# Optimization experiments

Hardware: AMD Instinct MI355X
Metric: run time of the kernel (lower is better)

## Reference

```python
import jax, jax.numpy as jnp
import numpy as np


def _conv(x, w, b, stride, pad):
    y = jax.lax.conv_general_dilated(
        x, w, (stride, stride), [(pad, pad), (pad, pad)],
        dimension_numbers=('NCHW', 'OIHW', 'NCHW'))
    return y + b[None, :, None, None]


def _maxpool(x):
    # kernel 3, stride 2, padding 1 (torch MaxPool2d semantics)
    return jax.lax.reduce_window(
        x, -jnp.inf, jax.lax.max,
        (1, 1, 3, 3), (1, 1, 2, 2), [(0, 0), (0, 0), (1, 1), (1, 1)])


def _squash(s, eps=1e-8):
    n2 = jnp.sum(s * s, axis=-1, keepdims=True)
    return s * (n2 / (1.0 + n2)) / jnp.sqrt(n2 + eps)


def setup_inputs() -> dict:
    key = jax.random.key(0)
    ks = jax.random.split(key, 17)
    s = 0.05
    inp = {
        'x': jax.random.normal(ks[0], (128, 3, 32, 32), jnp.float32),
        'cw1': jax.random.normal(ks[1], (96, 3, 3, 3), jnp.float32) * s,
        'cb1': jnp.zeros((96,), jnp.float32),
        'cw2': jax.random.normal(ks[2], (256, 96, 3, 3), jnp.float32) * s,
        'cb2': jnp.zeros((256,), jnp.float32),
        'cw3': jax.random.normal(ks[3], (384, 256, 3, 3), jnp.float32) * s,
        'cb3': jnp.zeros((384,), jnp.float32),
        'pw': jax.random.normal(ks[4], (256, 384, 3, 3), jnp.float32) * s,  # 32 caps * 8 dim
        'pb': jnp.zeros((256,), jnp.float32),
        'Wcaps': jax.random.normal(ks[5], (100, 1152, 16, 8), jnp.float32) * s,
        'fw1': jax.random.normal(ks[6], (1600, 4096), jnp.float32) * s,
        'fb1': jnp.zeros((4096,), jnp.float32),
        'fw2': jax.random.normal(ks[7], (4096, 4096), jnp.float32) * s,
        'fb2': jnp.zeros((4096,), jnp.float32),
        'fw3': jax.random.normal(ks[8], (4096, 100), jnp.float32) * s,
        'fb3': jnp.zeros((100,), jnp.float32),
    }
    return inp


def reference(x, cw1, cb1, cw2, cb2, cw3, cb3, pw, pb, Wcaps,
              fw1, fb1, fw2, fb2, fw3, fb3):
    ROUTINGS = 3
    # AlexNet-style conv backbone
    h = jax.nn.relu(_conv(x, cw1, cb1, 1, 1))   # [B,96,32,32]
    h = _maxpool(h)                              # [B,96,16,16]
    h = jax.nn.relu(_conv(h, cw2, cb2, 1, 1))   # [B,256,16,16]
    h = _maxpool(h)                              # [B,256,8,8]
    h = jax.nn.relu(_conv(h, cw3, cb3, 1, 1))   # [B,384,8,8]
    # PrimaryCaps: conv 384 -> 32*8, k3 s1 p0 -> [B,256,6,6]
    p = _conv(h, pw, pb, 1, 0)
    u = _squash(p.reshape(p.shape[0], -1, 8))   # [B,1152,8]
    # DenseCapsule: x_hat[b,o,i,d] = sum_e W[o,i,d,e] * u[b,i,e]
    x_hat = jnp.einsum('oide,bie->boid', Wcaps, u)  # [B,100,1152,16]
    x_hat_d = jax.lax.stop_gradient(x_hat)
    b = jnp.zeros(x_hat.shape[:3], x_hat.dtype)     # [B,100,1152]
    v = None
    for r in range(ROUTINGS):
        c = jax.nn.softmax(b, axis=1)               # couple over out caps
        if r == ROUTINGS - 1:
            v = _squash(jnp.einsum('boi,boid->bod', c, x_hat))
        else:
            v = _squash(jnp.einsum('boi,boid->bod', c, x_hat_d))
            b = b + jnp.einsum('boid,bod->boi', x_hat_d, v)
    # Flatten + FC head (dropout is identity at eval)
    f = v.reshape(v.shape[0], -1)                   # [B,1600]
    f = jax.nn.relu(f @ fw1 + fb1)
    f = jax.nn.relu(f @ fw2 + fb2)
    return f @ fw3 + fb3                            # [B,100]
```

## Files before the change

### kernel.cpp

```cpp
#include <hip/hip_runtime.h>
#include <cstddef>


typedef __attribute__((ext_vector_type(8))) short bf8_t;
typedef __attribute__((ext_vector_type(4))) float f4_t;

__device__ inline void cvt_hilo8(const float* f, unsigned* h, unsigned* l)
{
  #pragma unroll
  for (int j = 0; j < 4; ++j) {
    unsigned u0 = __float_as_uint(f[2 * j]);
    unsigned u1 = __float_as_uint(f[2 * j + 1]);
    h[j] = (u0 >> 16) | (u1 & 0xFFFF0000u);
    float r0 = f[2 * j]     - __uint_as_float(u0 & 0xFFFF0000u);
    float r1 = f[2 * j + 1] - __uint_as_float(u1 & 0xFFFF0000u);
    l[j] = (__float_as_uint(r0) >> 16) | (__float_as_uint(r1) & 0xFFFF0000u);
  }
}

__global__ __launch_bounds__(256) void conv1_k(
    const float* __restrict__ x, const float* __restrict__ wt,
    const float* __restrict__ bias, float* __restrict__ out)
{
  int idx = blockIdx.x * 256 + threadIdx.x;
  int w = idx & 31, h = (idx >> 5) & 31, b = idx >> 10;
  int co0 = blockIdx.y * 24;

  float xv[27];
  const float* xb = x + (size_t)b * 3072;
  #pragma unroll
  for (int ci = 0; ci < 3; ++ci)
    #pragma unroll
    for (int dh = 0; dh < 3; ++dh) {
      int ih = h + dh - 1;
      #pragma unroll
      for (int dw = 0; dw < 3; ++dw) {
        int iw = w + dw - 1;
        bool ok = ((unsigned)ih < 32u) & ((unsigned)iw < 32u);
        xv[ci * 9 + dh * 3 + dw] = ok ? xb[(ci << 10) + (ih << 5) + iw] : 0.f;
      }
    }

  float* op = out + (size_t)b * 98304 + ((size_t)co0 << 10) + (h << 5) + w;
  const float* wp = wt + (size_t)co0 * 27;
  #pragma unroll 2
  for (int co = 0; co < 24; ++co) {
    float acc = bias[co0 + co];
    #pragma unroll
    for (int k = 0; k < 27; ++k)
      acc += xv[k] * wp[co * 27 + k];
    op[(size_t)co << 10] = fmaxf(acc, 0.f);
  }
}

__global__ __launch_bounds__(256) void maxpool_k(
    const float* __restrict__ in, float* __restrict__ out, int H)
{
  int Ho = H >> 1;
  int idx = blockIdx.x * 256 + threadIdx.x;
  int wo = idx % Ho;
  int t2 = idx / Ho;
  int ho = t2 % Ho;
  int bc = t2 / Ho;
  const float* ip = in + (size_t)bc * H * H;
  float m = -3.4e38f;
  #pragma unroll
  for (int dh = 0; dh < 3; ++dh) {
    int ih = 2 * ho - 1 + dh;
    if (ih < 0 || ih >= H) continue;
    #pragma unroll
    for (int dw = 0; dw < 3; ++dw) {
      int iw = 2 * wo - 1 + dw;
      if (iw < 0 || iw >= H) continue;
      m = fmaxf(m, ip[ih * H + iw]);
    }
  }
  out[idx] = m;
}

template <int CI, int H, int PAD, int WO, bool SPLIT>
__global__ __launch_bounds__(256) void convgemm_mfma(
    const float* __restrict__ in, const float* __restrict__ wt,
    const float* __restrict__ bias, float* __restrict__ out,
    int CO, int relu, int KC)
{
  constexpr int K = CI * 9;
  constexpr int NPIX = WO * WO;
  __shared__ uint4 Ah[256], Al[256], Bh[256], Bl[256];
  int n0 = blockIdx.x * 64, m0 = blockIdx.y * 64;
  int kbeg = SPLIT ? blockIdx.z * KC : 0;
  int kend = SPLIT ? kbeg + KC : K;
  int t = threadIdx.x;
  int lane = t & 63;
  int wave = __builtin_amdgcn_readfirstlane(t >> 6);
  int wm = wave & 1, wn = wave >> 1;
  int lr = lane & 15, lq = lane >> 4;
  int smA = t >> 2, sgA = t & 3;

  int nn = n0 + lane;
  int bb = nn / NPIX, xy = nn - bb * NPIX;
  int ho = xy / WO, wo = xy - ho * WO;
  int ih0 = ho - PAD, iw0 = wo - PAD;
  const float* inb = in + (size_t)bb * CI * H * H;

  float fa[8], fb[8];
  auto loadA = [&](int k0) {
    const float4* ap = (const float4*)(wt + (size_t)(m0 + smA) * K + k0 + sgA * 8);
    float4 a0 = ap[0], a1 = ap[1];
    fa[0] = a0.x; fa[1] = a0.y; fa[2] = a0.z; fa[3] = a0.w;
    fa[4] = a1.x; fa[5] = a1.y; fa[6] = a1.z; fa[7] = a1.w;
  };
  auto loadB = [&](int k0) {
    int kb = k0 + wave * 8;
    int ci = kb / 9, rr = kb - ci * 9;
    int dh = rr / 3, dw = rr - dh * 3;
    #pragma unroll
    for (int j = 0; j < 8; ++j) {
      int ih = ih0 + dh, iw = iw0 + dw;
      bool ok = (ih >= 0 && ih < H && iw >= 0 && iw < H);
      fb[j] = ok ? inb[(ci * H + ih) * H + iw] : 0.f;
      if (++dw == 3) { dw = 0; if (++dh == 3) { dh = 0; ++ci; } }
    }
  };

  loadA(kbeg); loadB(kbeg);
  f4_t acc[2][2];
  #pragma unroll
  for (int mt = 0; mt < 2; ++mt)
    #pragma unroll
    for (int nt = 0; nt < 2; ++nt) acc[mt][nt] = (f4_t)0.0f;

  for (int k0 = kbeg; k0 < kend; k0 += 32) {
    if (k0 > kbeg) __syncthreads();
    unsigned ha[4], la[4], hb[4], lb[4];
    cvt_hilo8(fa, ha, la);
    cvt_hilo8(fb, hb, lb);
    Ah[sgA * 64 + smA] = make_uint4(ha[0], ha[1], ha[2], ha[3]);
    Al[sgA * 64 + smA] = make_uint4(la[0], la[1], la[2], la[3]);
    Bh[wave * 64 + lane] = make_uint4(hb[0], hb[1], hb[2], hb[3]);
    Bl[wave * 64 + lane] = make_uint4(lb[0], lb[1], lb[2], lb[3]);
    __syncthreads();
    if (k0 + 32 < kend) { loadA(k0 + 32); loadB(k0 + 32); }
    bf8_t av_h[2], av_l[2], bv_h[2], bv_l[2];
    #pragma unroll
    for (int mt = 0; mt < 2; ++mt) {
      int ui = lq * 64 + wm * 32 + mt * 16 + lr;
      av_h[mt] = *(const bf8_t*)&Ah[ui];
      av_l[mt] = *(const bf8_t*)&Al[ui];
    }
    #pragma unroll
    for (int nt = 0; nt < 2; ++nt) {
      int ui = lq * 64 + wn * 32 + nt * 16 + lr;
      bv_h[nt] = *(const bf8_t*)&Bh[ui];
      bv_l[nt] = *(const bf8_t*)&Bl[ui];
    }
    #pragma unroll
    for (int mt = 0; mt < 2; ++mt)
      #pragma unroll
      for (int nt = 0; nt < 2; ++nt) {
        acc[mt][nt] = __builtin_amdgcn_mfma_f32_16x16x32_bf16(av_h[mt], bv_h[nt], acc[mt][nt], 0, 0, 0);
        acc[mt][nt] = __builtin_amdgcn_mfma_f32_16x16x32_bf16(av_h[mt], bv_l[nt], acc[mt][nt], 0, 0, 0);
        acc[mt][nt] = __builtin_amdgcn_mfma_f32_16x16x32_bf16(av_l[mt], bv_h[nt], acc[mt][nt], 0, 0, 0);
      }
  }
  #pragma unroll
  for (int mt = 0; mt < 2; ++mt)
    #pragma unroll
    for (int nt = 0; nt < 2; ++nt) {
      #pragma unroll
      for (int r = 0; r < 4; ++r) {
        int m = m0 + wm * 32 + mt * 16 + lq * 4 + r;
        int n = n0 + wn * 32 + nt * 16 + lr;
        int b = n / NPIX, pxy = n - b * NPIX;
        size_t oidx = ((size_t)b * CO + m) * NPIX + pxy;
        if (SPLIT) {
          atomicAdd(out + oidx, acc[mt][nt][r]);
        } else {
          float vv = acc[mt][nt][r] + bias[m];
          if (relu) vv = fmaxf(vv, 0.f);
          out[oidx] = vv;
        }
      }
    }
}

__global__ __launch_bounds__(256) void fc_mfma(
    const float* __restrict__ A, const float* __restrict__ W,
    float* __restrict__ C, int K, int N, int KC)
{
  __shared__ uint4 Ah[256], Al[256], Bh[256], Bl[256];
  int n0 = blockIdx.x * 64, m0 = blockIdx.y * 64;
  int kbeg = blockIdx.z * KC, kend = kbeg + KC;
  int t = threadIdx.x;
  int lane = t & 63;
  int wave = __builtin_amdgcn_readfirstlane(t >> 6);
  int wm = wave & 1, wn = wave >> 1;
  int lr = lane & 15, lq = lane >> 4;
  int smA = t >> 2, sgA = t & 3;

  float fa[8], fb[8];
  auto loadA = [&](int k0) {
    const float4* ap = (const float4*)(A + (size_t)(m0 + smA) * K + k0 + sgA * 8);
    float4 a0 = ap[0], a1 = ap[1];
    fa[0] = a0.x; fa[1] = a0.y; fa[2] = a0.z; fa[3] = a0.w;
    fa[4] = a1.x; fa[5] = a1.y; fa[6] = a1.z; fa[7] = a1.w;
  };
  auto loadB = [&](int k0) {
    const float* wp = W + (size_t)(k0 + wave * 8) * N + n0 + lane;
    #pragma unroll
    for (int j = 0; j < 8; ++j) fb[j] = wp[(size_t)j * N];
  };

  loadA(kbeg); loadB(kbeg);
  f4_t acc[2][2];
  #pragma unroll
  for (int mt = 0; mt < 2; ++mt)
    #pragma unroll
    for (int nt = 0; nt < 2; ++nt) acc[mt][nt] = (f4_t)0.0f;

  for (int k0 = kbeg; k0 < kend; k0 += 32) {
    if (k0 > kbeg) __syncthreads();
    unsigned ha[4], la[4], hb[4], lb[4];
    cvt_hilo8(fa, ha, la);
    cvt_hilo8(fb, hb, lb);
    Ah[sgA * 64 + smA] = make_uint4(ha[0], ha[1], ha[2], ha[3]);
    Al[sgA * 64 + smA] = make_uint4(la[0], la[1], la[2], la[3]);
    Bh[wave * 64 + lane] = make_uint4(hb[0], hb[1], hb[2], hb[3]);
    Bl[wave * 64 + lane] = make_uint4(lb[0], lb[1], lb[2], lb[3]);
    __syncthreads();
    if (k0 + 32 < kend) { loadA(k0 + 32); loadB(k0 + 32); }
    bf8_t av_h[2], av_l[2], bv_h[2], bv_l[2];
    #pragma unroll
    for (int mt = 0; mt < 2; ++mt) {
      int ui = lq * 64 + wm * 32 + mt * 16 + lr;
      av_h[mt] = *(const bf8_t*)&Ah[ui];
      av_l[mt] = *(const bf8_t*)&Al[ui];
    }
    #pragma unroll
    for (int nt = 0; nt < 2; ++nt) {
      int ui = lq * 64 + wn * 32 + nt * 16 + lr;
      bv_h[nt] = *(const bf8_t*)&Bh[ui];
      bv_l[nt] = *(const bf8_t*)&Bl[ui];
    }
    #pragma unroll
    for (int mt = 0; mt < 2; ++mt)
      #pragma unroll
      for (int nt = 0; nt < 2; ++nt) {
        acc[mt][nt] = __builtin_amdgcn_mfma_f32_16x16x32_bf16(av_h[mt], bv_h[nt], acc[mt][nt], 0, 0, 0);
        acc[mt][nt] = __builtin_amdgcn_mfma_f32_16x16x32_bf16(av_h[mt], bv_l[nt], acc[mt][nt], 0, 0, 0);
        acc[mt][nt] = __builtin_amdgcn_mfma_f32_16x16x32_bf16(av_l[mt], bv_h[nt], acc[mt][nt], 0, 0, 0);
      }
  }
  #pragma unroll
  for (int mt = 0; mt < 2; ++mt)
    #pragma unroll
    for (int nt = 0; nt < 2; ++nt) {
      #pragma unroll
      for (int r = 0; r < 4; ++r) {
        int m = m0 + wm * 32 + mt * 16 + lq * 4 + r;
        int n = n0 + wn * 32 + nt * 16 + lr;
        atomicAdd(C + (size_t)m * N + n, acc[mt][nt][r]);
      }
    }
}

__global__ __launch_bounds__(256) void squash8_k(
    const float* __restrict__ p, const float* __restrict__ pb,
    float* __restrict__ ut)
{
  int idx = blockIdx.x * 256 + threadIdx.x;
  if (idx >= 147456) return;
  int b = idx & 127, i = idx >> 7;
  const float4* pp = (const float4*)(p + ((size_t)b * 1152 + i) * 8);
  float4 a = pp[0], bb = pp[1];
  float pv[8] = {a.x, a.y, a.z, a.w, bb.x, bb.y, bb.z, bb.w};
  int f0 = i * 8;
  #pragma unroll
  for (int e = 0; e < 8; ++e) pv[e] += pb[(f0 + e) / 36];
  float n2 = 0.f;
  #pragma unroll
  for (int e = 0; e < 8; ++e) n2 += pv[e] * pv[e];
  float sc = (n2 / (1.f + n2)) * rsqrtf(n2 + 1e-8f);
  #pragma unroll
  for (int e = 0; e < 8; ++e)
    ut[(size_t)i * 1024 + e * 128 + b] = pv[e] * sc;
}

__global__ __launch_bounds__(256) void caps_squash16(
    const float* __restrict__ s, float* __restrict__ v, float* __restrict__ vt)
{
  int idx = blockIdx.x * 256 + threadIdx.x;
  if (idx >= 12800) return;
  int b = idx / 100, o = idx % 100;
  const float4* sp = (const float4*)(s + (size_t)idx * 16);
  float4 a = sp[0], bb = sp[1], c = sp[2], d = sp[3];
  float n2 = a.x * a.x + a.y * a.y + a.z * a.z + a.w * a.w +
             bb.x * bb.x + bb.y * bb.y + bb.z * bb.z + bb.w * bb.w +
             c.x * c.x + c.y * c.y + c.z * c.z + c.w * c.w +
             d.x * d.x + d.y * d.y + d.z * d.z + d.w * d.w;
  float sc = (n2 / (1.f + n2)) * rsqrtf(n2 + 1e-8f);
  float vv[16] = {a.x, a.y, a.z, a.w, bb.x, bb.y, bb.z, bb.w,
                  c.x, c.y, c.z, c.w, d.x, d.y, d.z, d.w};
  float4* vp = (float4*)(v + (size_t)idx * 16);
  float4 o0 = {vv[0] * sc, vv[1] * sc, vv[2] * sc, vv[3] * sc};
  float4 o1 = {vv[4] * sc, vv[5] * sc, vv[6] * sc, vv[7] * sc};
  float4 o2 = {vv[8] * sc, vv[9] * sc, vv[10] * sc, vv[11] * sc};
  float4 o3 = {vv[12] * sc, vv[13] * sc, vv[14] * sc, vv[15] * sc};
  vp[0] = o0; vp[1] = o1; vp[2] = o2; vp[3] = o3;
  #pragma unroll
  for (int dd = 0; dd < 16; ++dd)
    vt[((size_t)o * 16 + dd) * 128 + b] = vv[dd] * sc;
}

__global__ __launch_bounds__(256) void caps_spass_mfma(
    const float* __restrict__ W, const float* __restrict__ ut,
    const float* __restrict__ ct, float* __restrict__ s, int uniform)
{
  __shared__ uint4 Ah[512], Al[512];
  int o = blockIdx.x, ks = blockIdx.y;
  int t = threadIdx.x;
  int lane = t & 63;
  int wave = __builtin_amdgcn_readfirstlane(t >> 6);
  int lr = lane & 15, lq = lane >> 4;
  int b = t & 127, half = t >> 7;
  int i0 = ks * 144;

  float fu[16], fc[2], fw[8];
  auto loadUC = [&](int j) {
    int ib = i0 + j * 4 + half * 2;
    #pragma unroll
    for (int q = 0; q < 2; ++q) {
      int i = ib + q;
      #pragma unroll
      for (int e = 0; e < 8; ++e)
        fu[q * 8 + e] = ut[(size_t)i * 1024 + e * 128 + b];
      fc[q] = uniform ? 0.01f : ct[((size_t)o * 1152 + i) * 128 + b];
    }
  };
  auto loadW = [&](int j) {
    int i = i0 + j * 4 + lq;
    const float4* wp = (const float4*)(W + (((size_t)o * 1152 + i) * 16 + lr) * 8);
    float4 w0 = wp[0], w1 = wp[1];
    fw[0] = w0.x; fw[1] = w0.y; fw[2] = w0.z; fw[3] = w0.w;
    fw[4] = w1.x; fw[5] = w1.y; fw[6] = w1.z; fw[7] = w1.w;
  };

  loadUC(0); loadW(0);
  f4_t acc[2];
  acc[0] = (f4_t)0.0f; acc[1] = (f4_t)0.0f;

  for (int j = 0; j < 36; ++j) {
    float cu[16];
    #pragma unroll
    for (int q = 0; q < 2; ++q)
      #pragma unroll
      for (int e = 0; e < 8; ++e)
        cu[q * 8 + e] = fc[q] * fu[q * 8 + e];
    unsigned h0[4], l0[4], h1[4], l1[4], wh[4], wl[4];
    cvt_hilo8(cu, h0, l0);
    cvt_hilo8(cu + 8, h1, l1);
    cvt_hilo8(fw, wh, wl);
    uint4 uwh = make_uint4(wh[0], wh[1], wh[2], wh[3]);
    uint4 uwl = make_uint4(wl[0], wl[1], wl[2], wl[3]);
    bf8_t bfh = *(const bf8_t*)&uwh;
    bf8_t bfl = *(const bf8_t*)&uwl;
    if (j > 0) __syncthreads();
    Ah[(half * 2 + 0) * 128 + b] = make_uint4(h0[0], h0[1], h0[2], h0[3]);
    Al[(half * 2 + 0) * 128 + b] = make_uint4(l0[0], l0[1], l0[2], l0[3]);
    Ah[(half * 2 + 1) * 128 + b] = make_uint4(h1[0], h1[1], h1[2], h1[3]);
    Al[(half * 2 + 1) * 128 + b] = make_uint4(l1[0], l1[1], l1[2], l1[3]);
    __syncthreads();
    if (j + 1 < 36) { loadUC(j + 1); loadW(j + 1); }
    #pragma unroll
    for (int mt = 0; mt < 2; ++mt) {
      int bidx = wave * 16 + mt * 64 + lr;
      bf8_t avh = *(const bf8_t*)&Ah[lq * 128 + bidx];
      bf8_t avl = *(const bf8_t*)&Al[lq * 128 + bidx];
      acc[mt] = __builtin_amdgcn_mfma_f32_16x16x32_bf16(avh, bfh, acc[mt], 0, 0, 0);
      acc[mt] = __builtin_amdgcn_mfma_f32_16x16x32_bf16(avh, bfl, acc[mt], 0, 0, 0);
      acc[mt] = __builtin_amdgcn_mfma_f32_16x16x32_bf16(avl, bfh, acc[mt], 0, 0, 0);
    }
  }
  #pragma unroll
  for (int mt = 0; mt < 2; ++mt)
    #pragma unroll
    for (int r = 0; r < 4; ++r) {
      int bb = wave * 16 + mt * 64 + lq * 4 + r;
      atomicAdd(s + ((size_t)bb * 100 + o) * 16 + lr, acc[mt][r]);
    }
}

__global__ __launch_bounds__(256) void caps_bupdate(
    const float* __restrict__ W, const float* __restrict__ ut,
    const float* __restrict__ vt, float* __restrict__ blogt, int accum)
{
  __shared__ __align__(16) float Wt[64 * 160];
  int o = blockIdx.x, ic = blockIdx.y;
  int t = threadIdx.x;
  int lane = t & 63;
  int wave = __builtin_amdgcn_readfirstlane(t >> 6);
  int lr = lane & 15, lq = lane >> 4;
  int dhalf = (lq & 1) << 3;
  int hl = lq >> 1;

  {
    const float4* Wg = (const float4*)(W + ((size_t)o * 1152 + (size_t)ic * 64) * 128);
    for (int l = t; l < 2048; l += 256) {
      float4 w = Wg[l];
      int li = l >> 5;
      int rem = l & 31;
      int d = rem >> 1;
      int e0 = (rem & 1) << 2;
      float* dst = &Wt[li * 160 + e0 * 20 + d];
      dst[0] = w.x; dst[20] = w.y; dst[40] = w.z; dst[60] = w.w;
    }
  }

  bf8_t B1[8], B2[8];
  #pragma unroll
  for (int nt = 0; nt < 8; ++nt) {
    int b = nt * 16 + lr;
    float vv[8];
    #pragma unroll
    for (int j = 0; j < 8; ++j)
      vv[j] = vt[((size_t)o * 16 + dhalf + j) * 128 + b];
    unsigned h[4], l2[4];
    cvt_hilo8(vv, h, l2);
    uint4 uh = make_uint4(h[0], h[1], h[2], h[3]);
    uint4 ul = (lq < 2) ? make_uint4(l2[0], l2[1], l2[2], l2[3])
                        : make_uint4(0u, 0u, 0u, 0u);
    B1[nt] = *(const bf8_t*)&uh;
    B2[nt] = *(const bf8_t*)&ul;
  }
  __syncthreads();

  unsigned lomask = hl ? 0xFFFF0000u : 0u;

  for (int mi = 0; mi < 8; ++mi) {
    int mt = wave * 8 + mi;
    int liA = mt * 2 + (lr >> 3);
    int eA = lr & 7;
    const float* wp = &Wt[liA * 160 + eA * 20 + dhalf];
    float4 wa = *(const float4*)wp;
    float4 wb = *(const float4*)(wp + 4);
    float fw[8] = {wa.x, wa.y, wa.z, wa.w, wb.x, wb.y, wb.z, wb.w};
    unsigned ha[4];
    #pragma unroll
    for (int j = 0; j < 4; ++j) {
      float f0 = fw[2 * j], f1 = fw[2 * j + 1];
      f0 -= __uint_as_float(__float_as_uint(f0) & lomask);
      f1 -= __uint_as_float(__float_as_uint(f1) & lomask);
      ha[j] = (__float_as_uint(f0) >> 16) | (__float_as_uint(f1) & 0xFFFF0000u);
    }
    uint4 ua = make_uint4(ha[0], ha[1], ha[2], ha[3]);
    bf8_t A = *(const bf8_t*)&ua;

    int gi = ic * 64 + mt * 2 + hl;
    const float* up = ut + (size_t)gi * 1024 + (size_t)(((lq & 1) << 2)) * 128;
    #pragma unroll
    for (int nt = 0; nt < 8; ++nt) {
      f4_t acc = (f4_t)0.0f;
      acc = __builtin_amdgcn_mfma_f32_16x16x32_bf16(A, B1[nt], acc, 0, 0, 0);
      acc = __builtin_amdgcn_mfma_f32_16x16x32_bf16(A, B2[nt], acc, 0, 0, 0);
      int b = nt * 16 + lr;
      float p = acc[0] * up[b] + acc[1] * up[128 + b] +
                acc[2] * up[256 + b] + acc[3] * up[384 + b];
      p += __shfl_xor(p, 16);
      if (!(lq & 1)) {
        size_t off = ((size_t)o * 1152 + gi) * 128 + b;
        if (accum) blogt[off] += p; else blogt[off] = p;
      }
    }
  }
}

__global__ __launch_bounds__(256) void caps_softmax(
    const float* __restrict__ blogt, float* __restrict__ ct)
{
  int idx = blockIdx.x * 256 + threadIdx.x;
  if (idx >= 147456) return;
  const float* bp = blogt + idx;
  float m = -3.4e38f;
  for (int o = 0; o < 100; ++o) m = fmaxf(m, bp[(size_t)o * 147456]);
  float sum = 0.f;
  for (int o = 0; o < 100; ++o) sum += __expf(bp[(size_t)o * 147456] - m);
  float inv = 1.f / sum;
  for (int o = 0; o < 100; ++o)
    ct[(size_t)o * 147456 + idx] = __expf(bp[(size_t)o * 147456] - m) * inv;
}

__global__ __launch_bounds__(256) void bias_act_k(
    float* __restrict__ C, const float* __restrict__ bias, int N, int total, int relu)
{
  int idx = blockIdx.x * 256 + threadIdx.x;
  if (idx >= total) return;
  float vv = C[idx] + bias[idx % N];
  if (relu) vv = fmaxf(vv, 0.f);
  C[idx] = vv;
}

__global__ __launch_bounds__(128) void fc3_seed(
    const float* __restrict__ bias, float* __restrict__ out)
{
  int idx = blockIdx.x * 128 + threadIdx.x;
  if (idx < 12800) out[idx] = bias[idx % 100];
}

__global__ __launch_bounds__(128) void fc3_sk(
    const float* __restrict__ A, const float* __restrict__ W,
    float* __restrict__ out)
{
  __shared__ float Al[1024];
  int m = blockIdx.x, z = blockIdx.y, t = threadIdx.x;
  int kbeg = z * 1024;
  const float* ap = A + (size_t)m * 4096 + kbeg;
  for (int l = t; l < 1024; l += 128) Al[l] = ap[l];
  __syncthreads();
  if (t < 100) {
    float acc = 0.f;
    const float* wp = W + (size_t)kbeg * 100 + t;
    #pragma unroll 8
    for (int k = 0; k < 1024; ++k) acc += Al[k] * wp[(size_t)k * 100];
    atomicAdd(out + m * 100 + t, acc);
  }
}

extern "C" void kernel_launch(void* const* d_in, const int* in_sizes, int n_in,
                              void* d_out, int out_size, void* d_ws, size_t ws_size,
                              hipStream_t stream)
{
  (void)in_sizes; (void)n_in; (void)out_size; (void)ws_size;
  const float* x   = (const float*)d_in[0];
  const float* cw1 = (const float*)d_in[1];
  const float* cb1 = (const float*)d_in[2];
  const float* cw2 = (const float*)d_in[3];
  const float* cb2 = (const float*)d_in[4];
  const float* cw3 = (const float*)d_in[5];
  const float* cb3 = (const float*)d_in[6];
  const float* pw  = (const float*)d_in[7];
  const float* pb  = (const float*)d_in[8];
  const float* Wc  = (const float*)d_in[9];
  const float* fw1 = (const float*)d_in[10];
  const float* fb1 = (const float*)d_in[11];
  const float* fw2 = (const float*)d_in[12];
  const float* fb2 = (const float*)d_in[13];
  const float* fw3 = (const float*)d_in[14];
  const float* fb3 = (const float*)d_in[15];
  float* ws = (float*)d_ws;

  const size_t OFF_A  = 0;
  const size_t OFF_B  = 12582912;
  const size_t OFF_U  = 15728640;
  const size_t OFF_P  = 16908288;
  const size_t OFF_C  = 18087936;
  const size_t OFF_V  = 32833536;
  const size_t OFF_S  = 33038336;
  const size_t OFF_F1 = 33243136;
  const size_t OFF_F2 = 33767424;

  float* A     = ws + OFF_A;
  float* Bf    = ws + OFF_B;
  float* ut    = ws + OFF_U;
  float* p     = ws + OFF_P;
  float* vt    = ws + OFF_P;
  float* ct    = ws + OFF_C;
  float* v     = ws + OFF_V;
  float* s     = ws + OFF_S;
  float* f1    = ws + OFF_F1;
  float* f2    = ws + OFF_F2;
  float* blogt = ws + OFF_A;

  hipMemsetAsync(p,  0, (size_t)1179648 * 4, stream);
  hipMemsetAsync(f1, 0, (size_t)524288 * 4, stream);
  hipMemsetAsync(f2, 0, (size_t)524288 * 4, stream);

  conv1_k<<<dim3(512, 4), 256, 0, stream>>>(x, cw1, cb1, A);
  maxpool_k<<<12288, 256, 0, stream>>>(A, Bf, 32);
  convgemm_mfma<96, 16, 1, 16, false><<<dim3(512, 4), 256, 0, stream>>>(Bf, cw2, cb2, A, 256, 1, 0);
  maxpool_k<<<8192, 256, 0, stream>>>(A, Bf, 16);
  convgemm_mfma<256, 8, 1, 8, false><<<dim3(128, 6), 256, 0, stream>>>(Bf, cw3, cb3, A, 384, 1, 0);
  convgemm_mfma<384, 8, 0, 6, true><<<dim3(72, 4, 2), 256, 0, stream>>>(A, pw, pb, p, 256, 0, 1728);
  squash8_k<<<576, 256, 0, stream>>>(p, pb, ut);

  for (int r = 0; r < 3; ++r) {
    hipMemsetAsync(s, 0, (size_t)204800 * 4, stream);
    if (r == 0) {
      caps_spass_mfma<<<dim3(100, 8), 256, 0, stream>>>(Wc, ut, ut , s, 1);
    } else {
      caps_softmax<<<576, 256, 0, stream>>>(blogt, ct);
      caps_spass_mfma<<<dim3(100, 8), 256, 0, stream>>>(Wc, ut, ct, s, 0);
    }
    caps_squash16<<<50, 256, 0, stream>>>(s, v, vt);
    if (r < 2)
      caps_bupdate<<<dim3(100, 18), 256, 0, stream>>>(Wc, ut, vt, blogt, r);
  }

  fc_mfma<<<dim3(64, 2, 2), 256, 0, stream>>>(v,  fw1, f1, 1600, 4096, 800);
  bias_act_k<<<2048, 256, 0, stream>>>(f1, fb1, 4096, 524288, 1);
  fc_mfma<<<dim3(64, 2, 4), 256, 0, stream>>>(f1, fw2, f2, 4096, 4096, 1024);
  bias_act_k<<<2048, 256, 0, stream>>>(f2, fb2, 4096, 524288, 1);
  fc3_seed<<<100, 128, 0, stream>>>(fb3, (float*)d_out);
  fc3_sk<<<dim3(128, 4), 128, 0, stream>>>(f2, fw3, (float*)d_out);
}
```

Before: 1.045 ms.

## Switch conv backbone to NHWC with pre-split bf16 hi/lo activations and weights

Conv activations are now stored in NHWC layout as separate bf16 high and low halves, and the conv weights are pre-split into hi/lo bf16 with a reordered K index of (tap, channel). Each conv GEMM can then load its A and B tiles with 16-byte vector loads instead of 8 scattered scalar loads, and it no longer converts fp32 to hi/lo in the inner loop. Maxpool and squash are adapted to the new layout. The cost is three extra weight-split kernels per call and a more complex epilogue that writes 2-byte hi/lo outputs.

```diff
diff --git a/kernel.cpp b/kernel.cpp
--- a/kernel.cpp
+++ b/kernel.cpp
@@ -18,9 +18,37 @@
   }
 }
 
+__device__ inline void split1(float f, unsigned short& h, unsigned short& l)
+{
+  unsigned u = __float_as_uint(f);
+  h = (unsigned short)(u >> 16);
+  float r = f - __uint_as_float(u & 0xFFFF0000u);
+  l = (unsigned short)(__float_as_uint(r) >> 16);
+}
+
+__device__ inline float bf2f(unsigned short h, unsigned short l)
+{
+  return __uint_as_float((unsigned)h << 16) + __uint_as_float((unsigned)l << 16);
+}
+
+__global__ __launch_bounds__(256) void wsplit_k(
+    const float* __restrict__ w, unsigned short* __restrict__ oh,
+    unsigned short* __restrict__ ol, int CO, int CI)
+{
+  int idx = blockIdx.x * 256 + threadIdx.x;
+  int ci = idx % CI;
+  int t2 = idx / CI;
+  int r = t2 % 9, co = t2 / 9;
+  float f = w[((size_t)co * CI + ci) * 9 + r];
+  unsigned short h, l;
+  split1(f, h, l);
+  oh[idx] = h; ol[idx] = l;
+}
+
 __global__ __launch_bounds__(256) void conv1_k(
     const float* __restrict__ x, const float* __restrict__ wt,
-    const float* __restrict__ bias, float* __restrict__ out)
+    const float* __restrict__ bias, unsigned short* __restrict__ oh,
+    unsigned short* __restrict__ ol)
 {
   int idx = blockIdx.x * 256 + threadIdx.x;
   int w = idx & 31, h = (idx >> 5) & 31, b = idx >> 10;
@@ -41,47 +69,61 @@
       }
     }
 
-  float* op = out + (size_t)b * 98304 + ((size_t)co0 << 10) + (h << 5) + w;
+  size_t obase = ((size_t)b * 1024 + (h << 5) + w) * 96 + co0;
   const float* wp = wt + (size_t)co0 * 27;
   #pragma unroll 2
-  for (int co = 0; co < 24; ++co) {
-    float acc = bias[co0 + co];
-    #pragma unroll
-    for (int k = 0; k < 27; ++k)
-      acc += xv[k] * wp[co * 27 + k];
-    op[(size_t)co << 10] = fmaxf(acc, 0.f);
-  }
-}
-
-__global__ __launch_bounds__(256) void maxpool_k(
-    const float* __restrict__ in, float* __restrict__ out, int H)
-{
-  int Ho = H >> 1;
+  for (int cp = 0; cp < 12; ++cp) {
+    float a0 = bias[co0 + 2 * cp], a1 = bias[co0 + 2 * cp + 1];
+    #pragma unroll
+    for (int k = 0; k < 27; ++k) {
+      a0 += xv[k] * wp[(2 * cp) * 27 + k];
+      a1 += xv[k] * wp[(2 * cp + 1) * 27 + k];
+    }
+    a0 = fmaxf(a0, 0.f); a1 = fmaxf(a1, 0.f);
+    unsigned short h0, l0, h1, l1;
+    split1(a0, h0, l0); split1(a1, h1, l1);
+    *(unsigned*)(oh + obase + 2 * cp) = (unsigned)h0 | ((unsigned)h1 << 16);
+    *(unsigned*)(ol + obase + 2 * cp) = (unsigned)l0 | ((unsigned)l1 << 16);
+  }
+}
+
+template <int C, int H>
+__global__ __launch_bounds__(256) void maxpool_bf(
+    const unsigned short* __restrict__ inh, const unsigned short* __restrict__ inl,
+    unsigned short* __restrict__ outh, unsigned short* __restrict__ outl)
+{
+  constexpr int Ho = H >> 1;
   int idx = blockIdx.x * 256 + threadIdx.x;
-  int wo = idx % Ho;
-  int t2 = idx / Ho;
-  int ho = t2 % Ho;
-  int bc = t2 / Ho;
-  const float* ip = in + (size_t)bc * H * H;
-  float m = -3.4e38f;
+  int c = idx % C;
+  int q = idx / C;
+  int wo = q % Ho;
+  int q2 = q / Ho;
+  int ho = q2 % Ho, b = q2 / Ho;
+  float best = -3.4e38f;
+  unsigned short bh = 0, bl = 0;
   #pragma unroll
   for (int dh = 0; dh < 3; ++dh) {
     int ih = 2 * ho - 1 + dh;
-    if (ih < 0 || ih >= H) continue;
+    if ((unsigned)ih >= (unsigned)H) continue;
     #pragma unroll
     for (int dw = 0; dw < 3; ++dw) {
       int iw = 2 * wo - 1 + dw;
-      if (iw < 0 || iw >= H) continue;
-      m = fmaxf(m, ip[ih * H + iw]);
-    }
-  }
-  out[idx] = m;
+      if ((unsigned)iw >= (unsigned)H) continue;
+      size_t off = ((size_t)(b * H + ih) * H + iw) * C + c;
+      unsigned short uh = inh[off], ul = inl[off];
+      float f = bf2f(uh, ul);
+      if (f > best) { best = f; bh = uh; bl = ul; }
+    }
+  }
+  outh[idx] = bh; outl[idx] = bl;
 }
 
 template <int CI, int H, int PAD, int WO, bool SPLIT>
-__global__ __launch_bounds__(256) void convgemm_mfma(
-    const float* __restrict__ in, const float* __restrict__ wt,
-    const float* __restrict__ bias, float* __restrict__ out,
+__global__ __launch_bounds__(256) void convgemm_nhwc(
+    const unsigned short* __restrict__ inh, const unsigned short* __restrict__ inl,
+    const unsigned short* __restrict__ wh, const unsigned short* __restrict__ wl,
+    const float* __restrict__ bias, unsigned short* __restrict__ outh,
+    unsigned short* __restrict__ outl, float* __restrict__ outf,
     int CO, int relu, int KC)
 {
   constexpr int K = CI * 9;
@@ -95,32 +137,117 @@
   int wave = __builtin_amdgcn_readfirstlane(t >> 6);
   int wm = wave & 1, wn = wave >> 1;
   int lr = lane & 15, lq = lane >> 4;
-  int smA = t >> 2, sgA = t & 3;
-
-  int nn = n0 + lane;
-  int bb = nn / NPIX, xy = nn - bb * NPIX;
+
+  int nn = m0 + lane;
+  int bpix = nn / NPIX, xy = nn - bpix * NPIX;
   int ho = xy / WO, wo = xy - ho * WO;
   int ih0 = ho - PAD, iw0 = wo - PAD;
-  const float* inb = in + (size_t)bb * CI * H * H;
+  size_t ibase = (size_t)bpix * H * H;
+
+  uint4 a_h, a_l, b_h, b_l;
+  auto loadA = [&](int k0) {
+    int kk = k0 + wave * 8;
+    int r = kk / CI, ci0 = kk - r * CI;
+    int dh = r / 3, dw = r - dh * 3;
+    int ih = ih0 + dh, iw = iw0 + dw;
+    bool ok = ((unsigned)ih < (unsigned)H) & ((unsigned)iw < (unsigned)H);
+    if (ok) {
+      size_t ad = ((ibase + (size_t)ih * H + iw) * CI + ci0);
+      a_h = *(const uint4*)(inh + ad);
+      a_l = *(const uint4*)(inl + ad);
+    } else {
+      a_h = make_uint4(0u, 0u, 0u, 0u);
+      a_l = make_uint4(0u, 0u, 0u, 0u);
+    }
+  };
+  auto loadB = [&](int k0) {
+    int kk = k0 + wave * 8;
+    size_t ad = (size_t)(n0 + lane) * K + kk;
+    b_h = *(const uint4*)(wh + ad);
+    b_l = *(const uint4*)(wl + ad);
+  };
+
+  loadA(kbeg); loadB(kbeg);
+  f4_t acc[2][2];
+  #pragma unroll
+  for (int mt = 0; mt < 2; ++mt)
+    #pragma unroll
+    for (int nt = 0; nt < 2; ++nt) acc[mt][nt] = (f4_t)0.0f;
+
+  for (int k0 = kbeg; k0 < kend; k0 += 32) {
+    if (k0 > kbeg) __syncthreads();
+    Ah[t] = a_h; Al[t] = a_l; Bh[t] = b_h; Bl[t] = b_l;
+    __syncthreads();
+    if (k0 + 32 < kend) { loadA(k0 + 32); loadB(k0 + 32); }
+    bf8_t av_h[2], av_l[2], bv_h[2], bv_l[2];
+    #pragma unroll
+    for (int mt = 0; mt < 2; ++mt) {
+      int ui = lq * 64 + wm * 32 + mt * 16 + lr;
+      av_h[mt] = *(const bf8_t*)&Ah[ui];
+      av_l[mt] = *(const bf8_t*)&Al[ui];
+    }
+    #pragma unroll
+    for (int nt = 0; nt < 2; ++nt) {
+      int ui = lq * 64 + wn * 32 + nt * 16 + lr;
+      bv_h[nt] = *(const bf8_t*)&Bh[ui];
+      bv_l[nt] = *(const bf8_t*)&Bl[ui];
+    }
+    #pragma unroll
+    for (int mt = 0; mt < 2; ++mt)
+      #pragma unroll
+      for (int nt = 0; nt < 2; ++nt) {
+        acc[mt][nt] = __builtin_amdgcn_mfma_f32_16x16x32_bf16(av_h[mt], bv_h[nt], acc[mt][nt], 0, 0, 0);
+        acc[mt][nt] = __builtin_amdgcn_mfma_f32_16x16x32_bf16(av_h[mt], bv_l[nt], acc[mt][nt], 0, 0, 0);
+        acc[mt][nt] = __builtin_amdgcn_mfma_f32_16x16x32_bf16(av_l[mt], bv_h[nt], acc[mt][nt], 0, 0, 0);
+      }
+  }
+  #pragma unroll
+  for (int mt = 0; mt < 2; ++mt)
+    #pragma unroll
+    for (int nt = 0; nt < 2; ++nt) {
+      #pragma unroll
+      for (int r = 0; r < 4; ++r) {
+        int m = m0 + wm * 32 + mt * 16 + lq * 4 + r;
+        int n = n0 + wn * 32 + nt * 16 + lr;
+        size_t oidx = (size_t)m * CO + n;
+        if (SPLIT) {
+          atomicAdd(outf + oidx, acc[mt][nt][r]);
+        } else {
+          float vv = acc[mt][nt][r] + bias[n];
+          if (relu) vv = fmaxf(vv, 0.f);
+          unsigned short h, l;
+          split1(vv, h, l);
+          outh[oidx] = h; outl[oidx] = l;
+        }
+      }
+    }
+}
+
+__global__ __launch_bounds__(256) void fc_mfma(
+    const float* __restrict__ A, const float* __restrict__ W,
+    float* __restrict__ C, int K, int N, int KC)
+{
+  __shared__ uint4 Ah[256], Al[256], Bh[256], Bl[256];
+  int n0 = blockIdx.x * 64, m0 = blockIdx.y * 64;
+  int kbeg = blockIdx.z * KC, kend = kbeg + KC;
+  int t = threadIdx.x;
+  int lane = t & 63;
+  int wave = __builtin_amdgcn_readfirstlane(t >> 6);
+  int wm = wave & 1, wn = wave >> 1;
+  int lr = lane & 15, lq = lane >> 4;
+  int smA = t >> 2, sgA = t & 3;
 
   float fa[8], fb[8];
   auto loadA = [&](int k0) {
-    const float4* ap = (const float4*)(wt + (size_t)(m0 + smA) * K + k0 + sgA * 8);
+    const float4* ap = (const float4*)(A + (size_t)(m0 + smA) * K + k0 + sgA * 8);
     float4 a0 = ap[0], a1 = ap[1];
     fa[0] = a0.x; fa[1] = a0.y; fa[2] = a0.z; fa[3] = a0.w;
     fa[4] = a1.x; fa[5] = a1.y; fa[6] = a1.z; fa[7] = a1.w;
   };
   auto loadB = [&](int k0) {
-    int kb = k0 + wave * 8;
-    int ci = kb / 9, rr = kb - ci * 9;
-    int dh = rr / 3, dw = rr - dh * 3;
-    #pragma unroll
-    for (int j = 0; j < 8; ++j) {
-      int ih = ih0 + dh, iw = iw0 + dw;
-      bool ok = (ih >= 0 && ih < H && iw >= 0 && iw < H);
-      fb[j] = ok ? inb[(ci * H + ih) * H + iw] : 0.f;
-      if (++dw == 3) { dw = 0; if (++dh == 3) { dh = 0; ++ci; } }
-    }
+    const float* wp = W + (size_t)(k0 + wave * 8) * N + n0 + lane;
+    #pragma unroll
+    for (int j = 0; j < 8; ++j) fb[j] = wp[(size_t)j * N];
   };
 
   loadA(kbeg); loadB(kbeg);
@@ -171,94 +298,6 @@
       for (int r = 0; r < 4; ++r) {
         int m = m0 + wm * 32 + mt * 16 + lq * 4 + r;
         int n = n0 + wn * 32 + nt * 16 + lr;
-        int b = n / NPIX, pxy = n - b * NPIX;
-        size_t oidx = ((size_t)b * CO + m) * NPIX + pxy;
-        if (SPLIT) {
-          atomicAdd(out + oidx, acc[mt][nt][r]);
-        } else {
-          float vv = acc[mt][nt][r] + bias[m];
-          if (relu) vv = fmaxf(vv, 0.f);
-          out[oidx] = vv;
-        }
-      }
-    }
-}
-
-__global__ __launch_bounds__(256) void fc_mfma(
-    const float* __restrict__ A, const float* __restrict__ W,
-    float* __restrict__ C, int K, int N, int KC)
-{
-  __shared__ uint4 Ah[256], Al[256], Bh[256], Bl[256];
-  int n0 = blockIdx.x * 64, m0 = blockIdx.y * 64;
-  int kbeg = blockIdx.z * KC, kend = kbeg + KC;
-  int t = threadIdx.x;
-  int lane = t & 63;
-  int wave = __builtin_amdgcn_readfirstlane(t >> 6);
-  int wm = wave & 1, wn = wave >> 1;
-  int lr = lane & 15, lq = lane >> 4;
-  int smA = t >> 2, sgA = t & 3;
-
-  float fa[8], fb[8];
-  auto loadA = [&](int k0) {
-    const float4* ap = (const float4*)(A + (size_t)(m0 + smA) * K + k0 + sgA * 8);
-    float4 a0 = ap[0], a1 = ap[1];
-    fa[0] = a0.x; fa[1] = a0.y; fa[2] = a0.z; fa[3] = a0.w;
-    fa[4] = a1.x; fa[5] = a1.y; fa[6] = a1.z; fa[7] = a1.w;
-  };
-  auto loadB = [&](int k0) {
-    const float* wp = W + (size_t)(k0 + wave * 8) * N + n0 + lane;
-    #pragma unroll
-    for (int j = 0; j < 8; ++j) fb[j] = wp[(size_t)j * N];
-  };
-
-  loadA(kbeg); loadB(kbeg);
-  f4_t acc[2][2];
-  #pragma unroll
-  for (int mt = 0; mt < 2; ++mt)
-    #pragma unroll
-    for (int nt = 0; nt < 2; ++nt) acc[mt][nt] = (f4_t)0.0f;
-
-  for (int k0 = kbeg; k0 < kend; k0 += 32) {
-    if (k0 > kbeg) __syncthreads();
-    unsigned ha[4], la[4], hb[4], lb[4];
-    cvt_hilo8(fa, ha, la);
-    cvt_hilo8(fb, hb, lb);
-    Ah[sgA * 64 + smA] = make_uint4(ha[0], ha[1], ha[2], ha[3]);
-    Al[sgA * 64 + smA] = make_uint4(la[0], la[1], la[2], la[3]);
-    Bh[wave * 64 + lane] = make_uint4(hb[0], hb[1], hb[2], hb[3]);
-    Bl[wave * 64 + lane] = make_uint4(lb[0], lb[1], lb[2], lb[3]);
-    __syncthreads();
-    if (k0 + 32 < kend) { loadA(k0 + 32); loadB(k0 + 32); }
-    bf8_t av_h[2], av_l[2], bv_h[2], bv_l[2];
-    #pragma unroll
-    for (int mt = 0; mt < 2; ++mt) {
-      int ui = lq * 64 + wm * 32 + mt * 16 + lr;
-      av_h[mt] = *(const bf8_t*)&Ah[ui];
-      av_l[mt] = *(const bf8_t*)&Al[ui];
-    }
-    #pragma unroll
-    for (int nt = 0; nt < 2; ++nt) {
-      int ui = lq * 64 + wn * 32 + nt * 16 + lr;
-      bv_h[nt] = *(const bf8_t*)&Bh[ui];
-      bv_l[nt] = *(const bf8_t*)&Bl[ui];
-    }
-    #pragma unroll
-    for (int mt = 0; mt < 2; ++mt)
-      #pragma unroll
-      for (int nt = 0; nt < 2; ++nt) {
-        acc[mt][nt] = __builtin_amdgcn_mfma_f32_16x16x32_bf16(av_h[mt], bv_h[nt], acc[mt][nt], 0, 0, 0);
-        acc[mt][nt] = __builtin_amdgcn_mfma_f32_16x16x32_bf16(av_h[mt], bv_l[nt], acc[mt][nt], 0, 0, 0);
-        acc[mt][nt] = __builtin_amdgcn_mfma_f32_16x16x32_bf16(av_l[mt], bv_h[nt], acc[mt][nt], 0, 0, 0);
-      }
-  }
-  #pragma unroll
-  for (int mt = 0; mt < 2; ++mt)
-    #pragma unroll
-    for (int nt = 0; nt < 2; ++nt) {
-      #pragma unroll
-      for (int r = 0; r < 4; ++r) {
-        int m = m0 + wm * 32 + mt * 16 + lq * 4 + r;
-        int n = n0 + wn * 32 + nt * 16 + lr;
         atomicAdd(C + (size_t)m * N + n, acc[mt][nt][r]);
       }
     }
@@ -271,12 +310,13 @@
   int idx = blockIdx.x * 256 + threadIdx.x;
   if (idx >= 147456) return;
   int b = idx & 127, i = idx >> 7;
-  const float4* pp = (const float4*)(p + ((size_t)b * 1152 + i) * 8);
-  float4 a = pp[0], bb = pp[1];
-  float pv[8] = {a.x, a.y, a.z, a.w, bb.x, bb.y, bb.z, bb.w};
-  int f0 = i * 8;
-  #pragma unroll
-  for (int e = 0; e < 8; ++e) pv[e] += pb[(f0 + e) / 36];
+  float pv[8];
+  #pragma unroll
+  for (int e = 0; e < 8; ++e) {
+    int f = i * 8 + e;
+    int co = f / 36, pix = f - co * 36;
+    pv[e] = p[((size_t)b * 36 + pix) * 256 + co] + pb[co];
+  }
   float n2 = 0.f;
   #pragma unroll
   for (int e = 0; e < 8; ++e) n2 += pv[e] * pv[e];
@@ -558,8 +598,6 @@
   const size_t OFF_F1 = 33243136;
   const size_t OFF_F2 = 33767424;
 
-  float* A     = ws + OFF_A;
-  float* Bf    = ws + OFF_B;
   float* ut    = ws + OFF_U;
   float* p     = ws + OFF_P;
   float* vt    = ws + OFF_P;
@@ -570,16 +608,41 @@
   float* f2    = ws + OFF_F2;
   float* blogt = ws + OFF_A;
 
+  unsigned short* h1h  = (unsigned short*)(ws + OFF_A);
+  unsigned short* h1l  = h1h + 12582912;
+  unsigned short* mp1h = (unsigned short*)(ws + OFF_B);
+  unsigned short* mp1l = mp1h + 3145728;
+  unsigned short* h2h  = (unsigned short*)(ws + OFF_A);
+  unsigned short* h2l  = h2h + 8388608;
+  unsigned short* mp2h = (unsigned short*)(ws + OFF_B);
+  unsigned short* mp2l = mp2h + 2097152;
+  unsigned short* h3h  = (unsigned short*)(ws + OFF_A);
+  unsigned short* h3l  = h3h + 3145728;
+
+  unsigned short* wc2h = (unsigned short*)(ws + OFF_C);
+  unsigned short* wc2l = wc2h + 221184;
+  unsigned short* wc3h = wc2l + 221184;
+  unsigned short* wc3l = wc3h + 884736;
+  unsigned short* pwth = wc3l + 884736;
+  unsigned short* pwtl = pwth + 884736;
+
   hipMemsetAsync(p,  0, (size_t)1179648 * 4, stream);
   hipMemsetAsync(f1, 0, (size_t)524288 * 4, stream);
   hipMemsetAsync(f2, 0, (size_t)524288 * 4, stream);
 
-  conv1_k<<<dim3(512, 4), 256, 0, stream>>>(x, cw1, cb1, A);
-  maxpool_k<<<12288, 256, 0, stream>>>(A, Bf, 32);
-  convgemm_mfma<96, 16, 1, 16, false><<<dim3(512, 4), 256, 0, stream>>>(Bf, cw2, cb2, A, 256, 1, 0);
-  maxpool_k<<<8192, 256, 0, stream>>>(A, Bf, 16);
-  convgemm_mfma<256, 8, 1, 8, false><<<dim3(128, 6), 256, 0, stream>>>(Bf, cw3, cb3, A, 384, 1, 0);
-  convgemm_mfma<384, 8, 0, 6, true><<<dim3(72, 4, 2), 256, 0, stream>>>(A, pw, pb, p, 256, 0, 1728);
+  wsplit_k<<<864, 256, 0, stream>>>(cw2, wc2h, wc2l, 256, 96);
+  wsplit_k<<<3456, 256, 0, stream>>>(cw3, wc3h, wc3l, 384, 256);
+  wsplit_k<<<3456, 256, 0, stream>>>(pw,  pwth, pwtl, 256, 384);
+
+  conv1_k<<<dim3(512, 4), 256, 0, stream>>>(x, cw1, cb1, h1h, h1l);
+  maxpool_bf<96, 32><<<12288, 256, 0, stream>>>(h1h, h1l, mp1h, mp1l);
+  convgemm_nhwc<96, 16, 1, 16, false><<<dim3(4, 512), 256, 0, stream>>>(
+      mp1h, mp1l, wc2h, wc2l, cb2, h2h, h2l, nullptr, 256, 1, 0);
+  maxpool_bf<256, 16><<<8192, 256, 0, stream>>>(h2h, h2l, mp2h, mp2l);
+  convgemm_nhwc<256, 8, 1, 8, false><<<dim3(6, 128), 256, 0, stream>>>(
+      mp2h, mp2l, wc3h, wc3l, cb3, h3h, h3l, nullptr, 384, 1, 0);
+  convgemm_nhwc<384, 8, 0, 6, true><<<dim3(4, 72, 2), 256, 0, stream>>>(
+      h3h, h3l, pwth, pwtl, pb, nullptr, nullptr, p, 256, 0, 1728);
   squash8_k<<<576, 256, 0, stream>>>(p, pb, ut);
 
   for (int r = 0; r < 3; ++r) {
```

Measured after the change: 1.131 ms. 8.2% more time.
